# Kernel optimization log

Hardware: AMD Instinct MI355X
Metric: run time of the kernel (lower is better)

The kernel has to match this reference:

```python
import jax, jax.numpy as jnp
import numpy as np

# Dims: B batch, CK key dim, CV value dim, NOBJ objects, T memory frames, HxW feature map
B, CK, CV, NOBJ, T, H, W = 1, 64, 512, 2, 2, 64, 64


def setup_inputs() -> dict:
    key = jax.random.key(0)
    k1, k2, k3, k4, k5 = jax.random.split(key, 5)
    return {
        "query_key": jax.random.normal(k1, (B, CK, H, W), jnp.float32),
        "query_selection": jax.random.uniform(k2, (B, CK, H, W), jnp.float32),
        "memory_key": jax.random.normal(k3, (B, CK, T, H, W), jnp.float32),
        "memory_shrinkage": jax.random.uniform(k4, (B, 1, T, H, W), jnp.float32),
        "memory_value": jax.random.normal(k5, (B, NOBJ, CV, T, H, W), jnp.float32),
    }


def reference(query_key, query_selection, memory_key, memory_shrinkage, memory_value):
    b, nobj, cv = memory_value.shape[:3]
    ck = memory_key.shape[1]
    h, w = query_key.shape[-2:]
    hw = h * w
    mk = memory_key.reshape(b, ck, -1)            # (b, ck, N) with N = T*H*W
    ms = memory_shrinkage.reshape(b, -1)          # (b, N)
    qk = query_key.reshape(b, ck, hw)             # (b, ck, hw)
    qe = query_selection.reshape(b, ck, hw)       # (b, ck, hw)
    mv = memory_value.reshape(b, nobj * cv, -1)   # (b, nobj*cv, N)

    # Negative L2 similarity with selection weighting (XMem get_similarity)
    a_sq = jnp.einsum('bcn,bcp->bnp', mk * mk, qe)            # (b, N, hw)
    two_ab = 2.0 * jnp.einsum('bcn,bcp->bnp', mk, qk * qe)    # (b, N, hw)
    b_sq = jnp.sum(qe * qk * qk, axis=1, keepdims=True)       # (b, 1, hw)
    inv_sqrt_ck = np.float32(1.0 / np.sqrt(ck))
    sim = (two_ab - a_sq - b_sq) * ms[:, :, None] * inv_sqrt_ck

    # Softmax over memory slots (dim N), then weighted readout
    aff = jax.nn.softmax(sim, axis=1)                          # (b, N, hw)
    mem = jnp.einsum('bvn,bnp->bvp', mv, aff)                  # (b, nobj*cv, hw)
    return mem.reshape(b, nobj, cv, h, w)
```

## Files before the change

### kernel.cpp

```cpp
#include <hip/hip_runtime.h>
#include <stdint.h>

typedef unsigned short u16;
typedef __attribute__((ext_vector_type(4))) float f32x4;
typedef __attribute__((ext_vector_type(8))) __bf16 bf16x8;
typedef __attribute__((ext_vector_type(4))) unsigned int u32x4;

#define HWPX 4096
#define NMEM 8192
#define CKD  64
#define VROWS 1024

__device__ __forceinline__ u16 f2bf(float x) {
    union { float f; unsigned u; } v; v.f = x;
    unsigned r = v.u + 0x7FFFu + ((v.u >> 16) & 1u);
    return (u16)(r >> 16);
}

__device__ __forceinline__ void gld_lds16(const void* g, void* l) {
    __builtin_amdgcn_global_load_lds(
        (const __attribute__((address_space(1))) uint32_t*)g,
        (__attribute__((address_space(3))) uint32_t*)l, 16, 0, 0);
}


__global__ void prep_aux(const float* __restrict__ qk, const float* __restrict__ qe,
                         const float* __restrict__ mk, const float* __restrict__ mv,
                         u16* __restrict__ Qf, float* __restrict__ bsq,
                         u16* __restrict__ Kf, u16* __restrict__ mvb,
                         float* __restrict__ outz) {
    const int bx = blockIdx.x;
    const int tid = threadIdx.x;
    if (bx < 16) {
        int p = bx * 256 + tid;
        const int pt = p >> 7, wm = (p >> 6) & 1, mi = (p >> 4) & 3, l15 = p & 15;
        const size_t cb = ((((size_t)pt * 2 + 0) * 2 + wm) * 4 + mi) * 2;
        float acc = 0.f;
        #pragma unroll
        for (int cg = 0; cg < 8; ++cg) {
            const int kk = cg >> 2, quad = cg & 3;
            float kv[8], ev[8];
            #pragma unroll
            for (int j = 0; j < 8; ++j) {
                int c = cg * 8 + j;
                kv[j] = qk[c * HWPX + p];
                ev[j] = qe[c * HWPX + p];
                acc += ev[j] * kv[j] * kv[j];
            }
            unsigned w0[4], w1[4];
            #pragma unroll
            for (int jj = 0; jj < 4; ++jj) {
                w0[jj] = (unsigned)f2bf(kv[2*jj] * ev[2*jj]) |
                         ((unsigned)f2bf(kv[2*jj+1] * ev[2*jj+1]) << 16);
                w1[jj] = (unsigned)f2bf(ev[2*jj]) |
                         ((unsigned)f2bf(ev[2*jj+1]) << 16);
            }
            const size_t off = (size_t)quad * 128 + (size_t)l15 * 8;
            *(u32x4*)(Qf + (cb + kk) * 512 + off)      = (u32x4){w0[0], w0[1], w0[2], w0[3]};
            *(u32x4*)(Qf + (cb + 16 + kk) * 512 + off) = (u32x4){w1[0], w1[1], w1[2], w1[3]};
        }
        bsq[p] = acc;
        return;
    }
    if (bx < 48) {
        int n = (bx - 16) * 256 + tid;
        const int nt = n >> 7, wn = (n >> 6) & 1, ni = (n >> 4) & 3, l15 = n & 15;
        const size_t cb = ((((size_t)nt * 2 + 0) * 2 + wn) * 4 + ni) * 2;
        #pragma unroll
        for (int cg = 0; cg < 8; ++cg) {
            const int kk = cg >> 2, quad = cg & 3;
            float m[8];
            #pragma unroll
            for (int j = 0; j < 8; ++j)
                m[j] = mk[(cg * 8 + j) * NMEM + n];
            unsigned w0[4], w1[4];
            #pragma unroll
            for (int jj = 0; jj < 4; ++jj) {
                w0[jj] = (unsigned)f2bf(2.f * m[2*jj]) |
                         ((unsigned)f2bf(2.f * m[2*jj+1]) << 16);
                w1[jj] = (unsigned)f2bf(-m[2*jj] * m[2*jj]) |
                         ((unsigned)f2bf(-m[2*jj+1] * m[2*jj+1]) << 16);
            }
            const size_t off = (size_t)quad * 128 + (size_t)l15 * 8;
            *(u32x4*)(Kf + (cb + kk) * 512 + off)      = (u32x4){w0[0], w0[1], w0[2], w0[3]};
            *(u32x4*)(Kf + (cb + 16 + kk) * 512 + off) = (u32x4){w1[0], w1[1], w1[2], w1[3]};
        }
        return;
    }
    if (bx < 560) {
        const int blk = bx - 48;
        #pragma unroll 4
        for (int it = 0; it < 16; ++it) {
            int i = blk * 4096 + it * 256 + tid;
            float4 v = ((const float4*)mv)[i];
            u16 o0 = f2bf(v.x), o1 = f2bf(v.y), o2 = f2bf(v.z), o3 = f2bf(v.w);
            unsigned lo = (unsigned)o0 | ((unsigned)o1 << 16);
            unsigned hi = (unsigned)o2 | ((unsigned)o3 << 16);
            ((uint2*)mvb)[i] = make_uint2(lo, hi);
        }
        return;
    }
    {
        const int blk = bx - 560;
        #pragma unroll 4
        for (int it = 0; it < 16; ++it) {
            int i = blk * 4096 + it * 256 + tid;
            ((float4*)outz)[i] = make_float4(0.f, 0.f, 0.f, 0.f);
        }
    }
}

__launch_bounds__(256, 2)
__global__ void gemm1_tiles(const u16* __restrict__ Qf, const u16* __restrict__ Kf,
                            const float* __restrict__ bsq, const float* __restrict__ ms,
                            u16* __restrict__ Pt, float* __restrict__ dpart) {
    __shared__ __align__(16) u16 smem[17408];

    const int tile = blockIdx.x;
    const int pb = tile & 31;
    const int nb = tile >> 5;
    const int p0 = pb * 128;
    const int n0 = nb * 128;

    const int tid  = threadIdx.x;
    const int l    = tid & 63;
    const int w    = tid >> 6;
    const int quad = l >> 4;
    const int l15  = l & 15;
    const int wm = w >> 1, wn = w & 1;

    f32x4 acc[4][4] = {};

    #pragma unroll
    for (int h = 0; h < 2; ++h) {
        bf16x8 a[4][2], b[4][2];
        const u16* qbase = Qf + ((((size_t)pb * 2 + h) * 2 + wm) * 4096) + (size_t)l * 8;
        const u16* kbase = Kf + ((((size_t)nb * 2 + h) * 2 + wn) * 4096) + (size_t)l * 8;
        #pragma unroll
        for (int mi = 0; mi < 4; ++mi) {
            a[mi][0] = *(const bf16x8*)(qbase + mi * 1024);
            a[mi][1] = *(const bf16x8*)(qbase + mi * 1024 + 512);
        }
        #pragma unroll
        for (int ni = 0; ni < 4; ++ni) {
            b[ni][0] = *(const bf16x8*)(kbase + ni * 1024);
            b[ni][1] = *(const bf16x8*)(kbase + ni * 1024 + 512);
        }
        #pragma unroll
        for (int kk = 0; kk < 2; ++kk)
            #pragma unroll
            for (int mi = 0; mi < 4; ++mi)
                #pragma unroll
                for (int ni = 0; ni < 4; ++ni)
                    acc[mi][ni] = __builtin_amdgcn_mfma_f32_16x16x32_bf16(a[mi][kk], b[ni][kk], acc[mi][ni], 0, 0, 0);
    }

    float msv[4];
    #pragma unroll
    for (int ni = 0; ni < 4; ++ni)
        msv[ni] = ms[n0 + wn * 64 + ni * 16 + l15] * 0.125f;
    float bsv[4][4];
    #pragma unroll
    for (int mi = 0; mi < 4; ++mi)
        #pragma unroll
        for (int r = 0; r < 4; ++r)
            bsv[mi][r] = bsq[p0 + wm * 64 + mi * 16 + quad * 4 + r];

    u16* Ps = smem;
    float rowsum[4][4] = {};
    #pragma unroll
    for (int mi = 0; mi < 4; ++mi) {
        #pragma unroll
        for (int ni = 0; ni < 4; ++ni) {
            f32x4 v = acc[mi][ni];
            int col = wn * 64 + ni * 16 + l15;
            #pragma unroll
            for (int r = 0; r < 4; ++r) {
                int rowl = wm * 64 + mi * 16 + quad * 4 + r;
                float pv = __expf((v[r] - bsv[mi][r]) * msv[ni]);
                rowsum[mi][r] += pv;
                Ps[rowl * 136 + col] = f2bf(pv);
            }
        }
    }
    #pragma unroll
    for (int mi = 0; mi < 4; ++mi)
        #pragma unroll
        for (int r = 0; r < 4; ++r) {
            float s = rowsum[mi][r];
            s += __shfl_xor(s, 1);
            s += __shfl_xor(s, 2);
            s += __shfl_xor(s, 4);
            s += __shfl_xor(s, 8);
            rowsum[mi][r] = s;
        }
    {
        float myv = 0.f;
        #pragma unroll
        for (int mi = 0; mi < 4; ++mi)
            #pragma unroll
            for (int r = 0; r < 4; ++r)
                if (l15 == mi * 4 + r) myv = rowsum[mi][r];
        int slice = nb * 2 + wn;
        dpart[(size_t)slice * HWPX + p0 + wm * 64 + (l15 >> 2) * 16 + quad * 4 + (l15 & 3)] = myv;
    }
    __syncthreads();

    {
        const size_t dstBase = (size_t)pb * 1048576 + (size_t)nb * 16384;
        #pragma unroll
        for (int it = 0; it < 8; ++it) {
            const int combo = it * 4 + w;
            const int kt  = combo >> 4;
            const int wnq = (combo >> 3) & 1;
            const int niq = (combo >> 1) & 3;
            const int kkq = combo & 1;
            const u32x4* src = (const u32x4*)(Ps + (wnq * 64 + niq * 16 + l15) * 136
                                                 + kt * 64 + kkq * 32 + quad * 8);
            u32x4* dst = (u32x4*)(Pt + dstBase + kt * 8192 + wnq * 4096
                                     + niq * 1024 + kkq * 512 + l * 8);
            *dst = *src;
        }
    }
}

__global__ void denom_kernel(const float* __restrict__ dpart, float* __restrict__ dinvg) {
    const int p = blockIdx.x * 256 + threadIdx.x;
    float s = 0.f;
    #pragma unroll 8
    for (int sl = 0; sl < 128; ++sl)
        s += dpart[(size_t)sl * HWPX + p];
    dinvg[p] = 1.0f / s;
}

__launch_bounds__(256, 4)
__global__ void gemm2_kernel(const u16* __restrict__ Ab, const u16* __restrict__ Btf,
                             const float* __restrict__ dinvg, float* __restrict__ outacc) {
    __shared__ __align__(16) u16 As[128 * 64];

    const int tid  = threadIdx.x;
    const int l    = tid & 63;
    const int w    = tid >> 6;
    const int quad = l >> 4;
    const int l15  = l & 15;
    const int wm = w >> 1, wn = w & 1;

    const int lin = blockIdx.x;
    const int pb  = (lin & 7) | ((lin >> 9) << 3);
    const int vb  = (lin >> 3) & 7;
    const int kz  = (lin >> 6) & 7;
    const int v0 = vb * 128;
    const int p0 = pb * 128;
    const int kbeg = kz * (NMEM / 8);

    const int rsub = tid >> 3;
    const int csw  = (tid & 7) ^ (rsub & 7);

    const u16* bbase = Btf + (size_t)pb * 1048576 + (size_t)wn * 4096 + (size_t)l * 8;

    f32x4 acc[4][4] = {};

    for (int t = 0; t < 16; ++t) {
        const int k0 = kbeg + t * 64;
        const int kt = k0 >> 6;
        __syncthreads();
        #pragma unroll
        for (int rnd = 0; rnd < 4; ++rnd)
            gld_lds16(Ab + (size_t)(v0 + rnd * 32 + rsub) * NMEM + k0 + csw * 8,
                      As + rnd * 2048 + w * 512);
        bf16x8 b[4][2];
        {
            const u16* bk = bbase + (size_t)kt * 8192;
            #pragma unroll
            for (int ni = 0; ni < 4; ++ni) {
                b[ni][0] = *(const bf16x8*)(bk + ni * 1024);
                b[ni][1] = *(const bf16x8*)(bk + ni * 1024 + 512);
            }
        }
        __syncthreads();
        #pragma unroll
        for (int kk = 0; kk < 2; ++kk) {
            bf16x8 a[4];
            #pragma unroll
            for (int mi = 0; mi < 4; ++mi) {
                int row = wm * 64 + mi * 16 + l15;
                a[mi] = *(const bf16x8*)(As + row * 64 + (((kk * 4 + quad) ^ (l15 & 7)) << 3));
            }
            #pragma unroll
            for (int mi = 0; mi < 4; ++mi)
                #pragma unroll
                for (int ni = 0; ni < 4; ++ni)
                    acc[mi][ni] = __builtin_amdgcn_mfma_f32_16x16x32_bf16(a[mi], b[ni][kk], acc[mi][ni], 0, 0, 0);
        }
    }

    float dinv[4];
    #pragma unroll
    for (int ni = 0; ni < 4; ++ni)
        dinv[ni] = dinvg[p0 + wn * 64 + ni * 16 + l15];

    #pragma unroll
    for (int mi = 0; mi < 4; ++mi) {
        #pragma unroll
        for (int ni = 0; ni < 4; ++ni) {
            int col = p0 + wn * 64 + ni * 16 + l15;
            f32x4 v = acc[mi][ni];
            #pragma unroll
            for (int r = 0; r < 4; ++r) {
                int row = v0 + wm * 64 + mi * 16 + quad * 4 + r;
                atomicAdd(&outacc[(size_t)row * HWPX + col], v[r] * dinv[ni]);
            }
        }
    }
}

extern "C" void kernel_launch(void* const* d_in, const int* in_sizes, int n_in,
                              void* d_out, int out_size, void* d_ws, size_t ws_size,
                              hipStream_t stream) {
    const float* qk = (const float*)d_in[0];
    const float* qe = (const float*)d_in[1];
    const float* mk = (const float*)d_in[2];
    const float* ms = (const float*)d_in[3];
    const float* mv = (const float*)d_in[4];
    float* out = (float*)d_out;

    char* ws = (char*)d_ws;
    u16*   Pt    = (u16*)ws;
    u16*   mvb   = (u16*)(ws + ((size_t)64 << 20));
    u16*   Kf    = (u16*)(ws + ((size_t)80 << 20));
    u16*   Qf    = (u16*)(ws + ((size_t)82 << 20));
    float* bsq   = (float*)(ws + ((size_t)83 << 20));
    float* dpart = (float*)(ws + ((size_t)83 << 20) + 65536);
    float* dinvg = (float*)(ws + ((size_t)83 << 20) + 65536 + (2 << 20));

    prep_aux<<<816, 256, 0, stream>>>(qk, qe, mk, mv, Qf, bsq, Kf, mvb, out);

    gemm1_tiles<<<2048, 256, 0, stream>>>(Qf, Kf, bsq, ms, Pt, dpart);

    denom_kernel<<<16, 256, 0, stream>>>(dpart, dinvg);

    gemm2_kernel<<<2048, 256, 0, stream>>>(mvb, Pt, dinvg, out);
}
```

Before: 268.4 us.

## Double-buffer gemm2 LDS and B registers, halve split-K count

Rewrites the gemm2 main loop so the A tile for the next step is staged into a second LDS buffer and the B fragments are prefetched into alternate registers, with explicit vmcnt waits and one barrier per step instead of two. It also cuts split-K from 8 to 4, giving each block 32 k-steps and halving the atomic writes to the output. MFMA sections get raised wave priority. The cost is double the LDS, more registers under the 4-blocks-per-CU bound, and fewer blocks (1024 instead of 2048) to spread across CUs.

```diff
diff --git a/kernel.cpp b/kernel.cpp
--- a/kernel.cpp
+++ b/kernel.cpp
@@ -236,7 +236,7 @@
 __launch_bounds__(256, 4)
 __global__ void gemm2_kernel(const u16* __restrict__ Ab, const u16* __restrict__ Btf,
                              const float* __restrict__ dinvg, float* __restrict__ outacc) {
-    __shared__ __align__(16) u16 As[128 * 64];
+    __shared__ __align__(16) u16 As2[2 * 8192];
 
     const int tid  = threadIdx.x;
     const int l    = tid & 63;
@@ -245,54 +245,78 @@
     const int l15  = l & 15;
     const int wm = w >> 1, wn = w & 1;
 
-    const int lin = blockIdx.x;
-    const int pb  = (lin & 7) | ((lin >> 9) << 3);
+    const int lin = blockIdx.x + (blockIdx.y << 3) + (blockIdx.z << 8);
     const int vb  = (lin >> 3) & 7;
-    const int kz  = (lin >> 6) & 7;
+    const int pb  = (lin & 7) | (((lin >> 6) & 3) << 3);
+    const int kz  = lin >> 8;
     const int v0 = vb * 128;
     const int p0 = pb * 128;
-    const int kbeg = kz * (NMEM / 8);
+    const int kbeg = kz * (NMEM / 4);
+    const int NT = 32;
 
     const int rsub = tid >> 3;
     const int csw  = (tid & 7) ^ (rsub & 7);
 
-    const u16* bbase = Btf + (size_t)pb * 1048576 + (size_t)wn * 4096 + (size_t)l * 8;
+    const u16* bbase = Btf + (size_t)pb * 1048576 + (size_t)wn * 4096 + (size_t)l * 8
+                           + (size_t)(kbeg >> 6) * 8192;
+
+    #define STAGE_A(t_, dst)                                                     \
+        { const int k0_ = kbeg + (t_) * 64;                                      \
+          _Pragma("unroll")                                                      \
+          for (int rnd = 0; rnd < 4; ++rnd)                                      \
+              gld_lds16(Ab + (size_t)(v0 + rnd * 32 + rsub) * NMEM + k0_ + csw * 8, \
+                        (dst) + rnd * 2048 + w * 512); }
+    #define LOADB(dst, t_)                                                       \
+        { const u16* bk_ = bbase + (size_t)(t_) * 8192;                          \
+          _Pragma("unroll")                                                      \
+          for (int ni = 0; ni < 4; ++ni) {                                       \
+              dst[ni][0] = *(const bf16x8*)(bk_ + ni * 1024);                    \
+              dst[ni][1] = *(const bf16x8*)(bk_ + ni * 1024 + 512);              \
+          } }
+    #define BODY(T, BC, BN)                                                      \
+    {   const int t_ = (T);                                                      \
+        if (t_ + 1 < NT) LOADB(BN, t_ + 1)                                       \
+        __builtin_amdgcn_sched_barrier(0);                                       \
+        if (t_ + 1 < NT) { asm volatile("s_waitcnt vmcnt(8)" ::: "memory"); }    \
+        else             { asm volatile("s_waitcnt vmcnt(0)" ::: "memory"); }    \
+        __builtin_amdgcn_s_barrier();                                            \
+        __builtin_amdgcn_sched_barrier(0);                                       \
+        if (t_ + 1 < NT) STAGE_A(t_ + 1, As2 + (((t_ + 1) & 1) * 8192))          \
+        const u16* rb_ = As2 + ((t_ & 1) * 8192);                                \
+        _Pragma("unroll")                                                        \
+        for (int kk = 0; kk < 2; ++kk) {                                         \
+            bf16x8 a_[4];                                                        \
+            _Pragma("unroll")                                                    \
+            for (int mi = 0; mi < 4; ++mi) {                                     \
+                int row_ = wm * 64 + mi * 16 + l15;                              \
+                a_[mi] = *(const bf16x8*)(rb_ + row_ * 64 + (((kk * 4 + quad) ^ (l15 & 7)) << 3)); \
+            }                                                                    \
+            __builtin_amdgcn_s_setprio(1);                                       \
+            _Pragma("unroll")                                                    \
+            for (int mi = 0; mi < 4; ++mi)                                       \
+                _Pragma("unroll")                                                \
+                for (int ni = 0; ni < 4; ++ni)                                   \
+                    acc[mi][ni] = __builtin_amdgcn_mfma_f32_16x16x32_bf16(       \
+                        a_[mi], BC[ni][kk], acc[mi][ni], 0, 0, 0);               \
+            __builtin_amdgcn_s_setprio(0);                                       \
+        }                                                                        \
+    }
 
     f32x4 acc[4][4] = {};
-
-    for (int t = 0; t < 16; ++t) {
-        const int k0 = kbeg + t * 64;
-        const int kt = k0 >> 6;
-        __syncthreads();
-        #pragma unroll
-        for (int rnd = 0; rnd < 4; ++rnd)
-            gld_lds16(Ab + (size_t)(v0 + rnd * 32 + rsub) * NMEM + k0 + csw * 8,
-                      As + rnd * 2048 + w * 512);
-        bf16x8 b[4][2];
-        {
-            const u16* bk = bbase + (size_t)kt * 8192;
-            #pragma unroll
-            for (int ni = 0; ni < 4; ++ni) {
-                b[ni][0] = *(const bf16x8*)(bk + ni * 1024);
-                b[ni][1] = *(const bf16x8*)(bk + ni * 1024 + 512);
-            }
-        }
-        __syncthreads();
-        #pragma unroll
-        for (int kk = 0; kk < 2; ++kk) {
-            bf16x8 a[4];
-            #pragma unroll
-            for (int mi = 0; mi < 4; ++mi) {
-                int row = wm * 64 + mi * 16 + l15;
-                a[mi] = *(const bf16x8*)(As + row * 64 + (((kk * 4 + quad) ^ (l15 & 7)) << 3));
-            }
-            #pragma unroll
-            for (int mi = 0; mi < 4; ++mi)
-                #pragma unroll
-                for (int ni = 0; ni < 4; ++ni)
-                    acc[mi][ni] = __builtin_amdgcn_mfma_f32_16x16x32_bf16(a[mi], b[ni][kk], acc[mi][ni], 0, 0, 0);
-        }
-    }
+    bf16x8 bX[4][2], bY[4][2];
+
+    LOADB(bX, 0)
+    __builtin_amdgcn_sched_barrier(0);
+    STAGE_A(0, As2)
+    __builtin_amdgcn_sched_barrier(0);
+
+    for (int t = 0; t < NT; t += 2) {
+        BODY(t,     bX, bY)
+        BODY(t + 1, bY, bX)
+    }
+    #undef BODY
+    #undef LOADB
+    #undef STAGE_A
 
     float dinv[4];
     #pragma unroll
@@ -339,5 +363,6 @@
 
     denom_kernel<<<16, 256, 0, stream>>>(dpart, dinvg);
 
-    gemm2_kernel<<<2048, 256, 0, stream>>>(mvb, Pt, dinvg, out);
-}
+    dim3 g2(8, 32, 4);
+    gemm2_kernel<<<g2, 256, 0, stream>>>(mvb, Pt, dinvg, out);
+}
```

After: 590.3 us. 120% more time.
